# Kernel optimization log

Hardware: AMD Instinct MI355X
Metric: run time of the kernel (lower is better)

Reference implementation:

```python
import jax, jax.numpy as jnp
import numpy as np

W = 128      # window_size
BACK = 1     # look_backward
FWD = 0      # look_forward (causal)


def _look_around(x, backward=BACK, forward=FWD, pad_value=-1):
    t = x.shape[1]
    pads = [(0, 0), (backward, forward)] + [(0, 0)] * (x.ndim - 2)
    p = jnp.pad(x, pads, constant_values=pad_value)
    return jnp.concatenate([p[:, i:i + t] for i in range(forward + backward + 1)], axis=2)


def setup_inputs() -> dict:
    key = jax.random.key(0)
    kq, kk, kv = jax.random.split(key, 3)
    B, H, T, D = 4, 8, 8192, 64
    q = jax.random.normal(kq, (B, H, T, D), jnp.float32)
    k = jax.random.normal(kk, (B, H, T, D), jnp.float32)
    v = jax.random.normal(kv, (B, H, T, D), jnp.float32)
    return {"q": q, "k": k, "v": v}


def reference(q, k, v):
    B, H, T, D = q.shape
    win = T // W
    # flatten batch/head, split into windows
    bq = q.reshape(B * H, win, W, D)
    bk = k.reshape(B * H, win, W, D)
    bv = v.reshape(B * H, win, W, D)
    bk = _look_around(bk)
    bv = _look_around(bv)

    bq_t = jnp.arange(T, dtype=jnp.int32).reshape(1, win, W)       # query positions
    bq_k = _look_around(bq_t, pad_value=-1)                        # key positions (pad = -1)

    scale = D ** -0.5
    dots = jnp.einsum('bwid,bwjd->bwij', bq, bk) * scale
    mask_value = -jnp.finfo(dots.dtype).max

    causal_mask = bq_t[:, :, :, None] < bq_k[:, :, None, :]
    pad_mask = (bq_k == -1)[:, :, None, :]
    dots = jnp.where(causal_mask | pad_mask, mask_value, dots)

    attn = jax.nn.softmax(dots, axis=-1)
    out = jnp.einsum('bwij,bwjd->bwid', attn, bv)
    return out.reshape(B, H, T, D)
```

## Files before the change

### kernel.cpp

```cpp
#include <hip/hip_runtime.h>
#include <hip/hip_bf16.h>

typedef __bf16 bf16x8 __attribute__((ext_vector_type(8)));
typedef float  f32x4  __attribute__((ext_vector_type(4)));
typedef float  f32x16 __attribute__((ext_vector_type(16)));
typedef unsigned int u32x4 __attribute__((ext_vector_type(4)));

#define TQ 8192
#define DD 64
#define PSTRV 264

static __device__ __forceinline__ unsigned pack2_bf16(float lo, float hi) {
    unsigned short a = __builtin_bit_cast(unsigned short, (__bf16)lo);
    unsigned short b = __builtin_bit_cast(unsigned short, (__bf16)hi);
    return ((unsigned)b << 16) | (unsigned)a;
}

static __device__ __forceinline__ int vt_idx(int d, int j) {
    return d * PSTRV + ((((j >> 3) ^ ((d >> 2) & 7)) << 3) | (j & 7));
}

__global__ __launch_bounds__(256, 4)
void lattn_kernel(const float* __restrict__ q, const float* __restrict__ k,
                  const float* __restrict__ v, float* __restrict__ out)
{
    __shared__ __align__(16) unsigned char smem[DD * PSTRV * 2];
    __bf16* Vt = (__bf16*)smem;
    float*  Ot = (float*)smem;

    const int bx0  = blockIdx.x;
    const int bx   = ((bx0 & 7) << 8) | (bx0 >> 3);
    const int bh   = bx >> 6;
    const int w    = bx & 63;
    const int tid  = threadIdx.x;
    const int lane = tid & 63;
    const int wv   = tid >> 6;
    const int l31  = lane & 31;
    const int hi   = lane >> 5;

    const size_t base  = ((size_t)bh * TQ + w * 128) * DD;
    const int    krow0 = w * 128 - 128;

    const int kb0   = (w == 0) ? 4 : 0;
    const int kbend = wv + 4;

    const float* kbase = k + ((size_t)bh * TQ + krow0) * DD + hi * 8;
    f32x4 kn[8];
    {
        const float* kp = kbase + (size_t)(kb0 * 32 + l31) * DD;
        #pragma unroll
        for (int s = 0; s < 4; ++s) {
            kn[2 * s]     = *(const f32x4*)(kp + 16 * s);
            kn[2 * s + 1] = *(const f32x4*)(kp + 16 * s + 4);
        }
    }

    bf16x8 qf[4];
    {
        const float* qp = q + base + (size_t)(wv * 32 + l31) * DD + hi * 8;
        #pragma unroll
        for (int s = 0; s < 4; ++s) {
            f32x4 a = *(const f32x4*)(qp + 16 * s);
            f32x4 b = *(const f32x4*)(qp + 16 * s + 4);
            #pragma unroll
            for (int e = 0; e < 4; ++e) { qf[s][e] = (__bf16)a[e]; qf[s][4 + e] = (__bf16)b[e]; }
        }
    }

    #pragma unroll
    for (int it = 0; it < 16; ++it) {
        int flat = it * 256 + tid;
        int j  = flat >> 4;
        int d0 = (flat & 15) * 4;
        int gr = krow0 + j;
        f32x4 val = {0.f, 0.f, 0.f, 0.f};
        if (gr >= 0) val = *(const f32x4*)(v + ((size_t)bh * TQ + gr) * DD + d0);
        #pragma unroll
        for (int c = 0; c < 4; ++c) Vt[vt_idx(d0 + c, j)] = (__bf16)val[c];
    }

    bf16x8 kf[4];
    #pragma unroll
    for (int s = 0; s < 4; ++s) {
        #pragma unroll
        for (int e = 0; e < 4; ++e) { kf[s][e] = (__bf16)kn[2 * s][e]; kf[s][4 + e] = (__bf16)kn[2 * s + 1][e]; }
    }
    __syncthreads();

    f32x16 o0 = {}, o1 = {};
    float m2 = -3.0e38f, lsum = 0.f;
    const float C = 0.18033688011112042f;

    for (int kb = kb0; kb <= kbend; ++kb) {
        if (kb < kbend) {
            const float* kp = kbase + (size_t)((kb + 1) * 32 + l31) * DD;
            #pragma unroll
            for (int s = 0; s < 4; ++s) {
                kn[2 * s]     = *(const f32x4*)(kp + 16 * s);
                kn[2 * s + 1] = *(const f32x4*)(kp + 16 * s + 4);
            }
        }

        f32x16 sacc = {};
        __builtin_amdgcn_s_setprio(1);
        #pragma unroll
        for (int s = 0; s < 4; ++s)
            sacc = __builtin_amdgcn_mfma_f32_32x32x16_bf16(kf[s], qf[s], sacc, 0, 0, 0);
        __builtin_amdgcn_s_setprio(0);

        float p[16];
        float locmax = -3.0e38f;
        const bool partial = (kb == kbend);
        #pragma unroll
        for (int r = 0; r < 16; ++r) {
            float sv = sacc[r] * C;
            int j = (r & 3) + 8 * (r >> 2) + 4 * hi;
            if (partial && (j > l31)) sv = -3.0e38f;
            p[r] = sv;
            locmax = fmaxf(locmax, sv);
        }
        locmax = fmaxf(locmax, __shfl_xor(locmax, 32, 64));
        float mnew = fmaxf(m2, locmax);
        float fac  = exp2f(m2 - mnew);
        float ts = 0.f;
        #pragma unroll
        for (int r = 0; r < 16; ++r) { float e = exp2f(p[r] - mnew); p[r] = e; ts += e; }
        ts += __shfl_xor(ts, 32, 64);
        lsum = lsum * fac + ts;
        m2 = mnew;
        #pragma unroll
        for (int r = 0; r < 16; ++r) { o0[r] *= fac; o1[r] *= fac; }

        unsigned pk[8], xw[8];
        #pragma unroll
        for (int m = 0; m < 8; ++m) pk[m] = pack2_bf16(p[2 * m], p[2 * m + 1]);
        #pragma unroll
        for (int m = 0; m < 8; ++m) xw[m] = (unsigned)__shfl_xor((int)pk[m], 32, 64);
        u32x4 f0, f1;
        f0[0] = hi ? xw[2] : pk[0]; f0[1] = hi ? xw[3] : pk[1];
        f0[2] = hi ? pk[2] : xw[0]; f0[3] = hi ? pk[3] : xw[1];
        f1[0] = hi ? xw[6] : pk[4]; f1[1] = hi ? xw[7] : pk[5];
        f1[2] = hi ? pk[6] : xw[4]; f1[3] = hi ? pk[7] : xw[5];
        bf16x8 pf0 = __builtin_bit_cast(bf16x8, f0);
        bf16x8 pf1 = __builtin_bit_cast(bf16x8, f1);

        const int jb = kb * 32 + hi * 8;
        bf16x8 v00 = *(const bf16x8*)&Vt[vt_idx(l31,      jb)];
        bf16x8 v01 = *(const bf16x8*)&Vt[vt_idx(l31,      jb + 16)];
        bf16x8 v10 = *(const bf16x8*)&Vt[vt_idx(l31 + 32, jb)];
        bf16x8 v11 = *(const bf16x8*)&Vt[vt_idx(l31 + 32, jb + 16)];
        __builtin_amdgcn_s_setprio(1);
        o0 = __builtin_amdgcn_mfma_f32_32x32x16_bf16(v00, pf0, o0, 0, 0, 0);
        o0 = __builtin_amdgcn_mfma_f32_32x32x16_bf16(v01, pf1, o0, 0, 0, 0);
        o1 = __builtin_amdgcn_mfma_f32_32x32x16_bf16(v10, pf0, o1, 0, 0, 0);
        o1 = __builtin_amdgcn_mfma_f32_32x32x16_bf16(v11, pf1, o1, 0, 0, 0);
        __builtin_amdgcn_s_setprio(0);

        #pragma unroll
        for (int s = 0; s < 4; ++s) {
            #pragma unroll
            for (int e = 0; e < 4; ++e) { kf[s][e] = (__bf16)kn[2 * s][e]; kf[s][4 + e] = (__bf16)kn[2 * s + 1][e]; }
        }
    }

    float rl = 1.0f / lsum;
    __syncthreads();
    {
        int iq = wv * 32 + l31;
        #pragma unroll
        for (int r = 0; r < 16; ++r) {
            int d = (r & 3) + 8 * (r >> 2) + 4 * hi;
            Ot[d * 132 + iq]        = o0[r] * rl;
            Ot[(d + 32) * 132 + iq] = o1[r] * rl;
        }
    }
    __syncthreads();
    {
        int iq = tid >> 1;
        int dh = (tid & 1) * 32;
        float* op = out + base + (size_t)iq * DD + dh;
        #pragma unroll
        for (int u = 0; u < 8; ++u) {
            f32x4 val;
            #pragma unroll
            for (int c = 0; c < 4; ++c) val[c] = Ot[(dh + u * 4 + c) * 132 + iq];
            *(f32x4*)(op + u * 4) = val;
        }
    }
}

extern "C" void kernel_launch(void* const* d_in, const int* in_sizes, int n_in,
                              void* d_out, int out_size, void* d_ws, size_t ws_size,
                              hipStream_t stream) {
    const float* q = (const float*)d_in[0];
    const float* k = (const float*)d_in[1];
    const float* v = (const float*)d_in[2];
    float* out = (float*)d_out;
    dim3 grid(32 * 64);
    dim3 block(256);
    lattn_kernel<<<grid, block, 0, stream>>>(q, k, v, out);
}
```

Measured before the change: 84.16 us.

## Process two adjacent windows per block to share the V tile in LDS

Each 512-thread block now handles two consecutive 128-query windows. The eight waves share one 384-row transposed V tile in LDS, since the windows overlap in their look-back keys, so each block loads 384 V rows where two separate blocks would have loaded 512. The output transpose is done in two phases through the same LDS buffer. LDS per block grows, and so do block size and the synchronization needed for the staged output writes, which may lower occupancy.

```diff
diff --git a/kernel.cpp b/kernel.cpp
--- a/kernel.cpp
+++ b/kernel.cpp
@@ -8,7 +8,7 @@
 
 #define TQ 8192
 #define DD 64
-#define PSTRV 264
+#define PSTRV 392
 
 static __device__ __forceinline__ unsigned pack2_bf16(float lo, float hi) {
     unsigned short a = __builtin_bit_cast(unsigned short, (__bf16)lo);
@@ -20,7 +20,7 @@
     return d * PSTRV + ((((j >> 3) ^ ((d >> 2) & 7)) << 3) | (j & 7));
 }
 
-__global__ __launch_bounds__(256, 4)
+__global__ __launch_bounds__(512, 4)
 void lattn_kernel(const float* __restrict__ q, const float* __restrict__ k,
                   const float* __restrict__ v, float* __restrict__ out)
 {
@@ -29,19 +29,22 @@
     float*  Ot = (float*)smem;
 
     const int bx0  = blockIdx.x;
-    const int bx   = ((bx0 & 7) << 8) | (bx0 >> 3);
-    const int bh   = bx >> 6;
-    const int w    = bx & 63;
+    const int bx   = ((bx0 & 7) << 7) | (bx0 >> 3);
+    const int bh   = bx >> 5;
+    const int wp   = bx & 31;
+    const int W0   = wp * 2;
     const int tid  = threadIdx.x;
     const int lane = tid & 63;
     const int wv   = tid >> 6;
+    const int wvw  = wv & 3;
     const int l31  = lane & 31;
     const int hi   = lane >> 5;
 
-    const size_t base  = ((size_t)bh * TQ + w * 128) * DD;
-    const int    krow0 = w * 128 - 128;
-
-    const int kb0   = (w == 0) ? 4 : 0;
+    const int win  = W0 + (wv >> 2);
+    const size_t base  = ((size_t)bh * TQ + win * 128) * DD;
+    const int    krow0 = W0 * 128 - 128;
+
+    const int kb0   = (wv < 4) ? ((W0 == 0) ? 4 : 0) : 4;
     const int kbend = wv + 4;
 
     const float* kbase = k + ((size_t)bh * TQ + krow0) * DD + hi * 8;
@@ -57,7 +60,7 @@
 
     bf16x8 qf[4];
     {
-        const float* qp = q + base + (size_t)(wv * 32 + l31) * DD + hi * 8;
+        const float* qp = q + base + (size_t)(wvw * 32 + l31) * DD + hi * 8;
         #pragma unroll
         for (int s = 0; s < 4; ++s) {
             f32x4 a = *(const f32x4*)(qp + 16 * s);
@@ -68,8 +71,8 @@
     }
 
     #pragma unroll
-    for (int it = 0; it < 16; ++it) {
-        int flat = it * 256 + tid;
+    for (int it = 0; it < 12; ++it) {
+        int flat = it * 512 + tid;
         int j  = flat >> 4;
         int d0 = (flat & 15) * 4;
         int gr = krow0 + j;
@@ -114,8 +117,8 @@
         #pragma unroll
         for (int r = 0; r < 16; ++r) {
             float sv = sacc[r] * C;
-            int j = (r & 3) + 8 * (r >> 2) + 4 * hi;
-            if (partial && (j > l31)) sv = -3.0e38f;
+            int jj = (r & 3) + 8 * (r >> 2) + 4 * hi;
+            if (partial && (jj > l31)) sv = -3.0e38f;
             p[r] = sv;
             locmax = fmaxf(locmax, sv);
         }
@@ -163,10 +166,13 @@
         }
     }
 
-    float rl = 1.0f / lsum;
-    __syncthreads();
-    {
-        int iq = wv * 32 + l31;
+    const float rl = 1.0f / lsum;
+    const int iq  = wvw * 32 + l31;
+    const int iq2 = tid >> 2;
+    const int dh  = (tid & 3) * 16;
+
+    __syncthreads();
+    if (wv < 4) {
         #pragma unroll
         for (int r = 0; r < 16; ++r) {
             int d = (r & 3) + 8 * (r >> 2) + 4 * hi;
@@ -176,14 +182,32 @@
     }
     __syncthreads();
     {
-        int iq = tid >> 1;
-        int dh = (tid & 1) * 32;
-        float* op = out + base + (size_t)iq * DD + dh;
-        #pragma unroll
-        for (int u = 0; u < 8; ++u) {
+        float* op = out + ((size_t)bh * TQ + W0 * 128) * DD + (size_t)iq2 * DD + dh;
+        #pragma unroll
+        for (int u = 0; u < 4; ++u) {
             f32x4 val;
             #pragma unroll
-            for (int c = 0; c < 4; ++c) val[c] = Ot[(dh + u * 4 + c) * 132 + iq];
+            for (int c = 0; c < 4; ++c) val[c] = Ot[(dh + u * 4 + c) * 132 + iq2];
+            *(f32x4*)(op + u * 4) = val;
+        }
+    }
+    __syncthreads();
+    if (wv >= 4) {
+        #pragma unroll
+        for (int r = 0; r < 16; ++r) {
+            int d = (r & 3) + 8 * (r >> 2) + 4 * hi;
+            Ot[d * 132 + iq]        = o0[r] * rl;
+            Ot[(d + 32) * 132 + iq] = o1[r] * rl;
+        }
+    }
+    __syncthreads();
+    {
+        float* op = out + ((size_t)bh * TQ + (W0 + 1) * 128) * DD + (size_t)iq2 * DD + dh;
+        #pragma unroll
+        for (int u = 0; u < 4; ++u) {
+            f32x4 val;
+            #pragma unroll
+            for (int c = 0; c < 4; ++c) val[c] = Ot[(dh + u * 4 + c) * 132 + iq2];
             *(f32x4*)(op + u * 4) = val;
         }
     }
@@ -196,7 +220,7 @@
     const float* k = (const float*)d_in[1];
     const float* v = (const float*)d_in[2];
     float* out = (float*)d_out;
-    dim3 grid(32 * 64);
-    dim3 block(256);
+    dim3 grid(32 * 32);
+    dim3 block(512);
     lattn_kernel<<<grid, block, 0, stream>>>(q, k, v, out);
 }
```

Result: slower. 86.57 us (+2.9%).
